# Kernel tuning notes

Hardware: AMD Instinct MI355X
Metric: run time of the kernel (lower is better)

## Reference

```python
import jax, jax.numpy as jnp
import numpy as np

B, S, D, H, V, DFF, L, MAXLEN = 256, 64, 1024, 16, 64, 4096, 8, 64
HD = D // H
SCALE = HD ** -0.5
EPS = 1e-5


def _ln(x, g, b):
    m = jnp.mean(x, axis=-1, keepdims=True)
    v = jnp.mean((x - m) ** 2, axis=-1, keepdims=True)
    return (x - m) * jax.lax.rsqrt(v + EPS) * g + b


def setup_inputs() -> dict:
    key = jax.random.key(0)
    ks = jax.random.split(key, 12)
    n = lambda k, shape: jax.random.normal(k, shape, jnp.float32) * 0.02
    return {
        "x": jax.random.randint(ks[0], (B, S), 0, V + 1),
        "step": 0,
        "token_embed": n(ks[1], (V + 1, D)),
        "step_embed": n(ks[2], (MAXLEN, D)),
        "qkv_w": n(ks[3], (L, 3 * D, D)),
        "qkv_b": jnp.zeros((L, 3 * D), jnp.float32),
        "out_w": n(ks[4], (L, D, D)),
        "out_b": jnp.zeros((L, D), jnp.float32),
        "rel_bias": n(ks[5], (L, 2 * MAXLEN - 1)),
        "w1": n(ks[6], (L, DFF, D)),
        "b1": jnp.zeros((L, DFF), jnp.float32),
        "w2": n(ks[7], (L, D, DFF)),
        "b2": jnp.zeros((L, D), jnp.float32),
        "ln1_g": jnp.ones((L, D), jnp.float32),
        "ln1_b": jnp.zeros((L, D), jnp.float32),
        "ln2_g": jnp.ones((L, D), jnp.float32),
        "ln2_b": jnp.zeros((L, D), jnp.float32),
        "lno_g": jnp.ones((D,), jnp.float32),
        "lno_b": jnp.zeros((D,), jnp.float32),
        "pol_w": n(ks[8], (V, D)),
        "pol_b": jnp.zeros((V,), jnp.float32),
        "val_w": n(ks[9], (1, D)),
        "val_b": jnp.zeros((1,), jnp.float32),
    }


def _forward(x, step, token_embed, step_embed, qkv_w, qkv_b, out_w, out_b,
             rel_bias, w1, b1, w2, b2, ln1_g, ln1_b, ln2_g, ln2_b,
             lno_g, lno_b, pol_w, pol_b, val_w, val_b):
    h = token_embed[x]  # [B,S,D]
    step_idx = min(int(step), MAXLEN - 1)
    h = h + step_embed[step_idx][None, None, :]

    pos = jnp.arange(S)
    rel_idx = jnp.clip(pos[:, None] - pos[None, :] + (MAXLEN - 1), 0, 2 * MAXLEN - 2)  # [S,S]

    def layer(h, p):
        qw, qb, ow, ob, rb, w1_, b1_, w2_, b2_, g1, be1, g2, be2 = p
        qkv = h @ qw.T + qb  # [B,S,3D]
        qkv = qkv.reshape(B, S, 3, H, HD).transpose(2, 0, 3, 1, 4)
        q, k, v = qkv[0], qkv[1], qkv[2]  # [B,H,S,HD]
        scores = jnp.einsum('bhqd,bhkd->bhqk', q, k) * SCALE + rb[rel_idx][None, None]
        probs = jax.nn.softmax(scores, axis=-1)
        attn = jnp.einsum('bhqk,bhkd->bhqd', probs, v)  # [B,H,S,HD]
        attn = attn.transpose(0, 2, 1, 3).reshape(B, S, D) @ ow.T + ob
        h = _ln(h + attn, g1, be1)
        ffn = jax.nn.gelu(h @ w1_.T + b1_, approximate=False) @ w2_.T + b2_
        h = _ln(h + ffn, g2, be2)
        return h, None

    h, _ = jax.lax.scan(layer, h, (qkv_w, qkv_b, out_w, out_b, rel_bias,
                                   w1, b1, w2, b2, ln1_g, ln1_b, ln2_g, ln2_b))
    h = _ln(h, lno_g, lno_b)
    pooled = h.mean(axis=1)  # [B,D]
    policy = pooled @ pol_w.T + pol_b  # [B,V]
    value = pooled @ val_w.T + val_b   # [B,1]
    return policy, value, h


def reference(x, step, token_embed, step_embed, qkv_w, qkv_b, out_w, out_b,
              rel_bias, w1, b1, w2, b2, ln1_g, ln1_b, ln2_g, ln2_b,
              lno_g, lno_b, pol_w, pol_b, val_w, val_b):
    return _forward(x, step, token_embed, step_embed, qkv_w, qkv_b, out_w, out_b,
                    rel_bias, w1, b1, w2, b2, ln1_g, ln1_b, ln2_g, ln2_b,
                    lno_g, lno_b, pol_w, pol_b, val_w, val_b)
```

## Files before the change

### kernel.cpp

```cpp
#include <hip/hip_runtime.h>
#include <math.h>

typedef _Float16 f16;
typedef _Float16 f16x8 __attribute__((ext_vector_type(8)));
typedef _Float16 f16x4 __attribute__((ext_vector_type(4)));
typedef float floatx4 __attribute__((ext_vector_type(4)));

#define BATCH 256
#define SEQ 64
#define DMODEL 1024
#define NHEAD 16
#define HDIM 64
#define VOCAB 64
#define DFF 4096
#define NLAYER 8
#define MS (BATCH*SEQ)

#define GPTR(p) ((const __attribute__((address_space(1))) void*)(p))
#define LPTR(p) ((__attribute__((address_space(3))) void*)(p))

__device__ __forceinline__ floatx4 mfma16(f16x8 a, f16x8 b, floatx4 c) {
    return __builtin_amdgcn_mfma_f32_16x16x32_f16(a, b, c, 0, 0, 0);
}

__device__ __forceinline__ float gelu_f(float x) {
    float x3 = x * x * x;
    float y = -1.5957691216f * fmaf(0.044715f, x3, x);
    return x / (1.f + __expf(y));
}

__global__ __launch_bounds__(256) void embed_k(const int* __restrict__ x, const int* __restrict__ step,
                                               const float* __restrict__ tok, const float* __restrict__ se,
                                               f16* __restrict__ r) {
    int row = blockIdx.x;
    int t = threadIdx.x;
    int id = x[row];
    int si = min(max(step[0], 0), 63);
    float4 a = ((const float4*)(tok + (size_t)id * DMODEL))[t];
    float4 b = ((const float4*)(se + (size_t)si * DMODEL))[t];
    f16x4 hv; hv[0] = (f16)(a.x + b.x); hv[1] = (f16)(a.y + b.y);
    hv[2] = (f16)(a.z + b.z); hv[3] = (f16)(a.w + b.w);
    ((f16x4*)(r + (size_t)row * DMODEL))[t] = hv;
}

__global__ __launch_bounds__(256) void cvt4_k(const float* __restrict__ qw, const float* __restrict__ ow,
                                              const float* __restrict__ w1, const float* __restrict__ w2,
                                              f16* __restrict__ dq, f16* __restrict__ dO,
                                              f16* __restrict__ d1, f16* __restrict__ d2) {
    int gid = blockIdx.x * 256 + threadIdx.x;
    const float4* s; f16x4* d; int off;
    if (gid < 786432)        { s = (const float4*)qw; d = (f16x4*)dq; off = gid; }
    else if (gid < 1048576)  { s = (const float4*)ow; d = (f16x4*)dO; off = gid - 786432; }
    else if (gid < 2097152)  { s = (const float4*)w1; d = (f16x4*)d1; off = gid - 1048576; }
    else                     { s = (const float4*)w2; d = (f16x4*)d2; off = gid - 2097152; }
    float4 v = s[off];
    f16x4 o; o[0] = (f16)v.x; o[1] = (f16)v.y; o[2] = (f16)v.z; o[3] = (f16)v.w;
    d[off] = o;
}

template<int MODE>
__global__ __launch_bounds__(256, 2) void gemm_k(const f16* __restrict__ A, const f16* __restrict__ Bw,
                                                 const float* __restrict__ bias,
                                                 f16* __restrict__ Cb,
                                                 const f16* __restrict__ Rres, f16* __restrict__ ResOut,
                                                 float2* __restrict__ Part,
                                                 int M, int N, int K) {
    __shared__ f16 smem[40960];

    const int tid = threadIdx.x;
    const int lane = tid & 63;
    const int wave = tid >> 6;
    const int wm = wave >> 1, wn = wave & 1;
    const int lr = lane & 15, lg = lane >> 4;
    const int sa = lr & 7;

    const unsigned nx = gridDim.x;
    const unsigned nwg = nx * gridDim.y;
    unsigned flat = blockIdx.y * nx + blockIdx.x;
    flat = (flat & 7u) * (nwg >> 3) + (flat >> 3);
    const int m0 = (int)(flat / nx) * 128;
    const int n0 = (int)(flat % nx) * 128;

    floatx4 acc[4][4] = {};

    const int srow = tid >> 3;
    const int scbs = (tid & 7) ^ (srow & 7);
    const f16* Asrc = A + (size_t)(m0 + srow) * K + scbs * 8;
    const f16* Bsrc = Bw + (size_t)(n0 + srow) * K + scbs * 8;
    const int ldsw = wave * 512;

#define STAGEA(bi, tt) do {                                                                       \
    const f16* _a = Asrc + (size_t)(tt) * 64;                                                     \
    f16* _l = smem + (bi) * 8192 + ldsw;                                                          \
    __builtin_amdgcn_global_load_lds(GPTR(_a),                  LPTR(_l),        16, 0, 0);       \
    __builtin_amdgcn_global_load_lds(GPTR(_a + 32 * (size_t)K), LPTR(_l + 2048), 16, 0, 0);       \
    __builtin_amdgcn_global_load_lds(GPTR(_a + 64 * (size_t)K), LPTR(_l + 4096), 16, 0, 0);       \
    __builtin_amdgcn_global_load_lds(GPTR(_a + 96 * (size_t)K), LPTR(_l + 6144), 16, 0, 0);       \
} while (0)

#define STAGEB(bi, tt) do {                                                                       \
    const f16* _b = Bsrc + (size_t)(tt) * 64;                                                     \
    f16* _l = smem + 16384 + (bi) * 8192 + ldsw;                                                  \
    __builtin_amdgcn_global_load_lds(GPTR(_b),                  LPTR(_l),        16, 0, 0);       \
    __builtin_amdgcn_global_load_lds(GPTR(_b + 32 * (size_t)K), LPTR(_l + 2048), 16, 0, 0);       \
    __builtin_amdgcn_global_load_lds(GPTR(_b + 64 * (size_t)K), LPTR(_l + 4096), 16, 0, 0);       \
    __builtin_amdgcn_global_load_lds(GPTR(_b + 96 * (size_t)K), LPTR(_l + 6144), 16, 0, 0);       \
} while (0)

    const int NT = K >> 6;

    STAGEA(0, 0);
    STAGEB(0, 0);
    STAGEB(1, 1);
    asm volatile("s_waitcnt vmcnt(4)" ::: "memory");
    __builtin_amdgcn_s_barrier();

    int ab = 0, bb = 0;
    for (int t = 0; t < NT; ++t) {
        if (t + 1 < NT) STAGEA(ab ^ 1, t + 1);
        if (t + 2 < NT) { int b2 = bb + 2; if (b2 >= 3) b2 -= 3; STAGEB(b2, t + 2); }

        const f16* Ab = smem + ab * 8192;
        const f16* Bb = smem + 16384 + bb * 8192;
        f16x8 af[8], bf[8];
#pragma unroll
        for (int kh = 0; kh < 2; ++kh)
#pragma unroll
            for (int mi = 0; mi < 4; ++mi)
                af[kh * 4 + mi] = *(const f16x8*)(Ab + (wm * 64 + mi * 16 + lr) * 64
                                                  + (((kh * 4 + lg) ^ sa) << 3));
#pragma unroll
        for (int kh = 0; kh < 2; ++kh)
#pragma unroll
            for (int ni = 0; ni < 4; ++ni)
                bf[kh * 4 + ni] = *(const f16x8*)(Bb + (wn * 64 + ni * 16 + lr) * 64
                                                  + (((kh * 4 + lg) ^ sa) << 3));

        __builtin_amdgcn_s_setprio(1);
#pragma unroll
        for (int kh = 0; kh < 2; ++kh)
#pragma unroll
            for (int mi = 0; mi < 4; ++mi)
#pragma unroll
                for (int ni = 0; ni < 4; ++ni)
                    acc[mi][ni] = mfma16(af[kh * 4 + mi], bf[kh * 4 + ni], acc[mi][ni]);
        __builtin_amdgcn_s_setprio(0);

        if (t + 2 < NT)      { asm volatile("s_waitcnt vmcnt(4)" ::: "memory"); }
        else if (t + 1 < NT) { asm volatile("s_waitcnt vmcnt(0)" ::: "memory"); }
        __builtin_amdgcn_s_barrier();

        ab ^= 1;
        bb = (bb == 2) ? 0 : bb + 1;
    }
#undef STAGEA
#undef STAGEB

    if (MODE == 2) {
        float bsv[4];
#pragma unroll
        for (int ni = 0; ni < 4; ++ni) bsv[ni] = bias[n0 + wn * 64 + ni * 16 + lr];
        f16* scr = smem + wave * 4096;
#pragma unroll
        for (int mi = 0; mi < 4; ++mi)
#pragma unroll
            for (int ni = 0; ni < 4; ++ni)
#pragma unroll
                for (int j = 0; j < 4; ++j) {
                    int rr = mi * 16 + lg * 4 + j;
                    int cc = ni * 16 + lr;
                    scr[rr * 64 + (((cc >> 3) ^ (rr & 7)) * 8) + (cc & 7)]
                        = (f16)(acc[mi][ni][j] + bsv[ni]);
                }
        int gr = m0 + wm * 64 + lane;
        const f16* rrow = Rres + (size_t)gr * N + n0 + wn * 64;
        f16* orow = ResOut + (size_t)gr * N + n0 + wn * 64;
        float s = 0.f, ss = 0.f;
#pragma unroll
        for (int i = 0; i < 8; ++i) {
            f16x8 a = *(const f16x8*)(scr + lane * 64 + ((i ^ (lane & 7)) * 8));
            f16x8 rv = *(const f16x8*)(rrow + i * 8);
            f16x8 o;
#pragma unroll
            for (int k = 0; k < 8; ++k) {
                float v = (float)a[k] + (float)rv[k];
                s += v; ss += v * v;
                o[k] = (f16)v;
            }
            *(f16x8*)(orow + i * 8) = o;
        }
        float* red = (float*)(smem + 16384);
        if (wn == 1) { red[(wm * 64 + lane) * 2] = s; red[(wm * 64 + lane) * 2 + 1] = ss; }
        __syncthreads();
        if (wn == 0) {
            float s2 = red[(wm * 64 + lane) * 2], ss2 = red[(wm * 64 + lane) * 2 + 1];
            Part[(size_t)gr * (N >> 7) + (n0 >> 7)] = float2{s + s2, ss + ss2};
        }
    } else {
        f16* scr = smem + wave * 4096;
        float bsv[4];
#pragma unroll
        for (int ni = 0; ni < 4; ++ni) bsv[ni] = bias[n0 + wn * 64 + ni * 16 + lr];
#pragma unroll
        for (int mi = 0; mi < 4; ++mi)
#pragma unroll
            for (int ni = 0; ni < 4; ++ni)
#pragma unroll
                for (int j = 0; j < 4; ++j) {
                    int rr = mi * 16 + lg * 4 + j;
                    int cc = ni * 16 + lr;
                    float v = acc[mi][ni][j] + bsv[ni];
                    if (MODE == 1) v = gelu_f(v);
                    scr[rr * 64 + (((cc >> 3) ^ (rr & 7)) * 8) + (cc & 7)] = (f16)v;
                }
        int gr = m0 + wm * 64 + lane;
        f16* dst = Cb + (size_t)gr * N + n0 + wn * 64;
#pragma unroll
        for (int i = 0; i < 8; ++i) {
            f16x8 v = *(const f16x8*)(scr + lane * 64 + ((i ^ (lane & 7)) * 8));
            *(f16x8*)(dst + i * 8) = v;
        }
    }
}

__global__ __launch_bounds__(64) void attn_k(const f16* __restrict__ qkv, const float* __restrict__ rb,
                                             f16* __restrict__ ctx) {
    const int hh = blockIdx.x;
    const int bb = blockIdx.y;
    const int lane = threadIdx.x;
    __shared__ float rbs[128];
    __shared__ f16 Vt[64][72];
    __shared__ f16 Pl[64][72];

    for (int i = lane; i < 127; i += 64) rbs[i] = rb[i];

    const f16* vrow = qkv + (size_t)(bb * 64 + lane) * 3072 + 2048 + hh * 64;
#pragma unroll
    for (int i = 0; i < 8; ++i) {
        f16x8 v = *(const f16x8*)(vrow + i * 8);
#pragma unroll
        for (int j = 0; j < 8; ++j) Vt[i * 8 + j][lane] = v[j];
    }
    __syncthreads();

    const int lr = lane & 15, lg = lane >> 4;
    floatx4 sacc[4][4] = {};
    const f16* qbase = qkv + (size_t)(bb * 64) * 3072 + hh * 64;
#pragma unroll
    for (int kk = 0; kk < 64; kk += 32) {
        f16x8 qa[4], kb[4];
#pragma unroll
        for (int mf = 0; mf < 4; ++mf)
            qa[mf] = *(const f16x8*)(qbase + (size_t)(mf * 16 + lr) * 3072 + kk + lg * 8);
#pragma unroll
        for (int nf = 0; nf < 4; ++nf)
            kb[nf] = *(const f16x8*)(qbase + 1024 + (size_t)(nf * 16 + lr) * 3072 + kk + lg * 8);
#pragma unroll
        for (int mf = 0; mf < 4; ++mf)
#pragma unroll
            for (int nf = 0; nf < 4; ++nf)
                sacc[mf][nf] = mfma16(qa[mf], kb[nf], sacc[mf][nf]);
    }

#pragma unroll
    for (int mf = 0; mf < 4; ++mf) {
#pragma unroll
        for (int j = 0; j < 4; ++j) {
            int qrow = mf * 16 + lg * 4 + j;
            float v0 = sacc[mf][0][j] * 0.125f + rbs[qrow - (0  + lr) + 63];
            float v1 = sacc[mf][1][j] * 0.125f + rbs[qrow - (16 + lr) + 63];
            float v2 = sacc[mf][2][j] * 0.125f + rbs[qrow - (32 + lr) + 63];
            float v3 = sacc[mf][3][j] * 0.125f + rbs[qrow - (48 + lr) + 63];
            float mx = fmaxf(fmaxf(v0, v1), fmaxf(v2, v3));
            for (int m = 1; m < 16; m <<= 1) mx = fmaxf(mx, __shfl_xor(mx, m));
            v0 = __expf(v0 - mx); v1 = __expf(v1 - mx); v2 = __expf(v2 - mx); v3 = __expf(v3 - mx);
            float sum = v0 + v1 + v2 + v3;
            for (int m = 1; m < 16; m <<= 1) sum += __shfl_xor(sum, m);
            float inv = 1.f / sum;
            Pl[qrow][0  + lr] = (f16)(v0 * inv);
            Pl[qrow][16 + lr] = (f16)(v1 * inv);
            Pl[qrow][32 + lr] = (f16)(v2 * inv);
            Pl[qrow][48 + lr] = (f16)(v3 * inv);
        }
    }
    __syncthreads();

    floatx4 oacc[4][4] = {};
#pragma unroll
    for (int kk = 0; kk < 64; kk += 32) {
        f16x8 pa[4], vb[4];
#pragma unroll
        for (int mf = 0; mf < 4; ++mf) pa[mf] = *(const f16x8*)&Pl[mf * 16 + lr][kk + lg * 8];
#pragma unroll
        for (int nf = 0; nf < 4; ++nf) vb[nf] = *(const f16x8*)&Vt[nf * 16 + lr][kk + lg * 8];
#pragma unroll
        for (int mf = 0; mf < 4; ++mf)
#pragma unroll
            for (int nf = 0; nf < 4; ++nf)
                oacc[mf][nf] = mfma16(pa[mf], vb[nf], oacc[mf][nf]);
    }
    __syncthreads();
#pragma unroll
    for (int mf = 0; mf < 4; ++mf)
#pragma unroll
        for (int nf = 0; nf < 4; ++nf)
#pragma unroll
            for (int j = 0; j < 4; ++j)
                Pl[mf * 16 + lg * 4 + j][nf * 16 + lr] = (f16)oacc[mf][nf][j];
    __syncthreads();
    f16* crow = ctx + (size_t)(bb * 64 + lane) * DMODEL + hh * 64;
#pragma unroll
    for (int i = 0; i < 8; ++i) {
        f16x8 v = *(const f16x8*)&Pl[lane][i * 8];
        *(f16x8*)(crow + i * 8) = v;
    }
}

__global__ __launch_bounds__(128) void ln_k(const f16* __restrict__ res, const float2* __restrict__ part,
                                            const float* __restrict__ g, const float* __restrict__ b,
                                            f16* __restrict__ out) {
    int row = blockIdx.x;
    int t = threadIdx.x;
    f16x8 rv = ((const f16x8*)(res + (size_t)row * DMODEL))[t];
    float s = 0.f, ss = 0.f;
#pragma unroll
    for (int c = 0; c < 8; ++c) {
        float2 p = part[(size_t)row * 8 + c];
        s += p.x; ss += p.y;
    }
    float mean = s * (1.f / 1024.f);
    float var = ss * (1.f / 1024.f) - mean * mean;
    float rstd = rsqrtf(var + 1e-5f);
    float4 g0 = ((const float4*)g)[t * 2], g1 = ((const float4*)g)[t * 2 + 1];
    float4 b0 = ((const float4*)b)[t * 2], b1 = ((const float4*)b)[t * 2 + 1];
    f16x8 o;
    o[0] = (f16)(((float)rv[0] - mean) * rstd * g0.x + b0.x);
    o[1] = (f16)(((float)rv[1] - mean) * rstd * g0.y + b0.y);
    o[2] = (f16)(((float)rv[2] - mean) * rstd * g0.z + b0.z);
    o[3] = (f16)(((float)rv[3] - mean) * rstd * g0.w + b0.w);
    o[4] = (f16)(((float)rv[4] - mean) * rstd * g1.x + b1.x);
    o[5] = (f16)(((float)rv[5] - mean) * rstd * g1.y + b1.y);
    o[6] = (f16)(((float)rv[6] - mean) * rstd * g1.z + b1.z);
    o[7] = (f16)(((float)rv[7] - mean) * rstd * g1.w + b1.w);
    ((f16x8*)(out + (size_t)row * DMODEL))[t] = o;
}

__global__ __launch_bounds__(256) void lnf_k(const f16* __restrict__ res, const float* __restrict__ g,
                                             const float* __restrict__ b, float* __restrict__ h) {
    int row = blockIdx.x;
    int t = threadIdx.x;
    f16x4 rv = ((const f16x4*)(res + (size_t)row * DMODEL))[t];
    float v0 = (float)rv[0], v1 = (float)rv[1], v2 = (float)rv[2], v3 = (float)rv[3];
    float s = v0 + v1 + v2 + v3;
    float ss = v0 * v0 + v1 * v1 + v2 * v2 + v3 * v3;
    for (int m = 1; m < 64; m <<= 1) { s += __shfl_xor(s, m); ss += __shfl_xor(ss, m); }
    __shared__ float red[8];
    if ((t & 63) == 0) { red[(t >> 6) * 2] = s; red[(t >> 6) * 2 + 1] = ss; }
    __syncthreads();
    s = red[0] + red[2] + red[4] + red[6];
    ss = red[1] + red[3] + red[5] + red[7];
    float mean = s * (1.f / 1024.f);
    float var = ss * (1.f / 1024.f) - mean * mean;
    float rstd = rsqrtf(var + 1e-5f);
    float4 gg = ((const float4*)g)[t];
    float4 bb = ((const float4*)b)[t];
    float4 o;
    o.x = (v0 - mean) * rstd * gg.x + bb.x;
    o.y = (v1 - mean) * rstd * gg.y + bb.y;
    o.z = (v2 - mean) * rstd * gg.z + bb.z;
    o.w = (v3 - mean) * rstd * gg.w + bb.w;
    ((float4*)(h + (size_t)row * DMODEL))[t] = o;
}

__global__ __launch_bounds__(256) void pool_k(const float* __restrict__ h, float* __restrict__ pooled) {
    int b = blockIdx.x;
    int t = threadIdx.x;
    float sx = 0, sy = 0, sz = 0, sw = 0;
    for (int s = 0; s < SEQ; ++s) {
        float4 v = ((const float4*)(h + (size_t)(b * SEQ + s) * DMODEL))[t];
        sx += v.x; sy += v.y; sz += v.z; sw += v.w;
    }
    float4 o; o.x = sx * (1.f / 64.f); o.y = sy * (1.f / 64.f); o.z = sz * (1.f / 64.f); o.w = sw * (1.f / 64.f);
    ((float4*)(pooled + (size_t)b * DMODEL))[t] = o;
}

__global__ __launch_bounds__(64) void head_k(const float* __restrict__ pooled, const float* __restrict__ pw,
                                             const float* __restrict__ pb, const float* __restrict__ vw,
                                             const float* __restrict__ vb, float* __restrict__ out) {
    int b = blockIdx.x;
    int lane = threadIdx.x;
    const float* pr = pooled + (size_t)b * DMODEL;
    const float* wr = pw + (size_t)lane * DMODEL;
    float accp = 0.f;
    for (int d = 0; d < DMODEL; d += 4) {
        float4 x = *(const float4*)(pr + d);
        float4 w = *(const float4*)(wr + d);
        accp += x.x * w.x + x.y * w.y + x.z * w.z + x.w * w.w;
    }
    float accv = 0.f;
    for (int d = lane * 4; d < DMODEL; d += 256) {
        float4 x = *(const float4*)(pr + d);
        float4 w = *(const float4*)(vw + d);
        accv += x.x * w.x + x.y * w.y + x.z * w.z + x.w * w.w;
    }
    for (int m = 1; m < 64; m <<= 1) accv += __shfl_xor(accv, m);
    out[b * VOCAB + lane] = accp + pb[lane];
    if (lane == 0) out[BATCH * VOCAB + b] = accv + vb[0];
}

extern "C" void kernel_launch(void* const* d_in, const int* in_sizes, int n_in,
                              void* d_out, int out_size, void* d_ws, size_t ws_size,
                              hipStream_t stream) {
    const int*   x      = (const int*)d_in[0];
    const int*   step   = (const int*)d_in[1];
    const float* tok    = (const float*)d_in[2];
    const float* se     = (const float*)d_in[3];
    const float* qkv_w  = (const float*)d_in[4];
    const float* qkv_b  = (const float*)d_in[5];
    const float* out_w  = (const float*)d_in[6];
    const float* out_b  = (const float*)d_in[7];
    const float* relb   = (const float*)d_in[8];
    const float* w1     = (const float*)d_in[9];
    const float* b1     = (const float*)d_in[10];
    const float* w2     = (const float*)d_in[11];
    const float* b2     = (const float*)d_in[12];
    const float* ln1g   = (const float*)d_in[13];
    const float* ln1b   = (const float*)d_in[14];
    const float* ln2g   = (const float*)d_in[15];
    const float* ln2b   = (const float*)d_in[16];
    const float* lnog   = (const float*)d_in[17];
    const float* lnob   = (const float*)d_in[18];
    const float* pw     = (const float*)d_in[19];
    const float* pb     = (const float*)d_in[20];
    const float* vw     = (const float*)d_in[21];
    const float* vb     = (const float*)d_in[22];

    float* out = (float*)d_out;
    float* h = out + BATCH * VOCAB + BATCH;

    char* ws = (char*)d_ws;
    f16* rB     = (f16*)(ws);
    f16* resA   = (f16*)(ws + 33554432);
    f16* qkv16  = (f16*)(ws + 67108864);
    f16* ctx16  = (f16*)(ws + 167772160);
    f16* ffn16  = (f16*)(ws + 67108864);
    f16* wqb    = (f16*)(ws + 201326592);
    f16* wob    = (f16*)(ws + 207618048);
    f16* w1b    = (f16*)(ws + 209715200);
    f16* w2b    = (f16*)(ws + 218103808);
    float2* part = (float2*)(ws + 226492416);
    float* pooled = (float*)(ws + 226492416);

    embed_k<<<MS, 256, 0, stream>>>(x, step, tok, se, rB);

    for (int l = 0; l < NLAYER; ++l) {
        cvt4_k<<<12288, 256, 0, stream>>>(qkv_w + (size_t)l * 3145728, out_w + (size_t)l * 1048576,
                                          w1 + (size_t)l * 4194304, w2 + (size_t)l * 4194304,
                                          wqb, wob, w1b, w2b);

        gemm_k<0><<<dim3(24, 128), 256, 0, stream>>>(rB, wqb, qkv_b + l * 3072, qkv16,
                                                     nullptr, nullptr, nullptr, MS, 3072, 1024);
        attn_k<<<dim3(NHEAD, BATCH), 64, 0, stream>>>(qkv16, relb + l * 127, ctx16);
        gemm_k<2><<<dim3(8, 128), 256, 0, stream>>>(ctx16, wob, out_b + l * 1024, nullptr,
                                                    rB, resA, part, MS, 1024, 1024);
        ln_k<<<MS, 128, 0, stream>>>(resA, part, ln1g + l * 1024, ln1b + l * 1024, rB);
        gemm_k<1><<<dim3(32, 128), 256, 0, stream>>>(rB, w1b, b1 + l * 4096, ffn16,
                                                     nullptr, nullptr, nullptr, MS, 4096, 1024);
        gemm_k<2><<<dim3(8, 128), 256, 0, stream>>>(ffn16, w2b, b2 + l * 1024, nullptr,
                                                    rB, resA, part, MS, 1024, 4096);
        ln_k<<<MS, 128, 0, stream>>>(resA, part, ln2g + l * 1024, ln2b + l * 1024, rB);
    }

    lnf_k<<<MS, 256, 0, stream>>>(rB, lnog, lnob, h);
    pool_k<<<BATCH, 256, 0, stream>>>(h, pooled);
    head_k<<<BATCH, 64, 0, stream>>>(pooled, pw, pb, vw, vb, out);
}
```

Baseline: 4.920 ms.

## Switch GEMM to 256x128 tiles with K=32 steps and unified triple-buffered staging

```diff
diff --git a/kernel.cpp b/kernel.cpp
--- a/kernel.cpp
+++ b/kernel.cpp
@@ -65,104 +65,84 @@
                                                  const f16* __restrict__ Rres, f16* __restrict__ ResOut,
                                                  float2* __restrict__ Part,
                                                  int M, int N, int K) {
-    __shared__ f16 smem[40960];
+    __shared__ f16 smem[36864];
 
     const int tid = threadIdx.x;
     const int lane = tid & 63;
     const int wave = tid >> 6;
     const int wm = wave >> 1, wn = wave & 1;
     const int lr = lane & 15, lg = lane >> 4;
-    const int sa = lr & 7;
+    const int sa = (lr ^ (lr >> 2)) & 3;
 
     const unsigned nx = gridDim.x;
     const unsigned nwg = nx * gridDim.y;
     unsigned flat = blockIdx.y * nx + blockIdx.x;
     flat = (flat & 7u) * (nwg >> 3) + (flat >> 3);
-    const int m0 = (int)(flat / nx) * 128;
+    const int m0 = (int)(flat / nx) * 256;
     const int n0 = (int)(flat % nx) * 128;
 
-    floatx4 acc[4][4] = {};
-
-    const int srow = tid >> 3;
-    const int scbs = (tid & 7) ^ (srow & 7);
-    const f16* Asrc = A + (size_t)(m0 + srow) * K + scbs * 8;
-    const f16* Bsrc = Bw + (size_t)(n0 + srow) * K + scbs * 8;
+    floatx4 acc[8][4] = {};
+
+    const int srow = tid >> 2;
+    const int lblk = (tid & 3) ^ ((srow ^ (srow >> 2)) & 3);
+    const f16* AsrcT = A + (size_t)(m0 + srow) * K + lblk * 8;
+    const f16* BsrcT = Bw + (size_t)(n0 + srow) * K + lblk * 8;
     const int ldsw = wave * 512;
 
-#define STAGEA(bi, tt) do {                                                                       \
-    const f16* _a = Asrc + (size_t)(tt) * 64;                                                     \
-    f16* _l = smem + (bi) * 8192 + ldsw;                                                          \
-    __builtin_amdgcn_global_load_lds(GPTR(_a),                  LPTR(_l),        16, 0, 0);       \
-    __builtin_amdgcn_global_load_lds(GPTR(_a + 32 * (size_t)K), LPTR(_l + 2048), 16, 0, 0);       \
-    __builtin_amdgcn_global_load_lds(GPTR(_a + 64 * (size_t)K), LPTR(_l + 4096), 16, 0, 0);       \
-    __builtin_amdgcn_global_load_lds(GPTR(_a + 96 * (size_t)K), LPTR(_l + 6144), 16, 0, 0);       \
+#define STAGE(bi, tt) do {                                                                        \
+    const f16* _a = AsrcT + (size_t)(tt) * 32;                                                    \
+    const f16* _b = BsrcT + (size_t)(tt) * 32;                                                    \
+    f16* _l = smem + (bi) * 12288 + ldsw;                                                         \
+    __builtin_amdgcn_global_load_lds(GPTR(_a),                   LPTR(_l),         16, 0, 0);     \
+    __builtin_amdgcn_global_load_lds(GPTR(_a +  64 * (size_t)K), LPTR(_l + 2048),  16, 0, 0);     \
+    __builtin_amdgcn_global_load_lds(GPTR(_a + 128 * (size_t)K), LPTR(_l + 4096),  16, 0, 0);     \
+    __builtin_amdgcn_global_load_lds(GPTR(_a + 192 * (size_t)K), LPTR(_l + 6144),  16, 0, 0);     \
+    __builtin_amdgcn_global_load_lds(GPTR(_b),                   LPTR(_l + 8192),  16, 0, 0);     \
+    __builtin_amdgcn_global_load_lds(GPTR(_b +  64 * (size_t)K), LPTR(_l + 10240), 16, 0, 0);     \
 } while (0)
 
-#define STAGEB(bi, tt) do {                                                                       \
-    const f16* _b = Bsrc + (size_t)(tt) * 64;                                                     \
-    f16* _l = smem + 16384 + (bi) * 8192 + ldsw;                                                  \
-    __builtin_amdgcn_global_load_lds(GPTR(_b),                  LPTR(_l),        16, 0, 0);       \
-    __builtin_amdgcn_global_load_lds(GPTR(_b + 32 * (size_t)K), LPTR(_l + 2048), 16, 0, 0);       \
-    __builtin_amdgcn_global_load_lds(GPTR(_b + 64 * (size_t)K), LPTR(_l + 4096), 16, 0, 0);       \
-    __builtin_amdgcn_global_load_lds(GPTR(_b + 96 * (size_t)K), LPTR(_l + 6144), 16, 0, 0);       \
-} while (0)
-
-    const int NT = K >> 6;
-
-    STAGEA(0, 0);
-    STAGEB(0, 0);
-    STAGEB(1, 1);
-    asm volatile("s_waitcnt vmcnt(4)" ::: "memory");
-    __builtin_amdgcn_s_barrier();
-
-    int ab = 0, bb = 0;
+    const int NT = K >> 5;
+
+    STAGE(0, 0);
+    STAGE(1, 1);
+
+    int buf = 0;
     for (int t = 0; t < NT; ++t) {
-        if (t + 1 < NT) STAGEA(ab ^ 1, t + 1);
-        if (t + 2 < NT) { int b2 = bb + 2; if (b2 >= 3) b2 -= 3; STAGEB(b2, t + 2); }
-
-        const f16* Ab = smem + ab * 8192;
-        const f16* Bb = smem + 16384 + bb * 8192;
-        f16x8 af[8], bf[8];
-#pragma unroll
-        for (int kh = 0; kh < 2; ++kh)
-#pragma unroll
-            for (int mi = 0; mi < 4; ++mi)
-                af[kh * 4 + mi] = *(const f16x8*)(Ab + (wm * 64 + mi * 16 + lr) * 64
-                                                  + (((kh * 4 + lg) ^ sa) << 3));
-#pragma unroll
-        for (int kh = 0; kh < 2; ++kh)
+        if (t + 1 < NT) { asm volatile("s_waitcnt vmcnt(6)" ::: "memory"); }
+        else            { asm volatile("s_waitcnt vmcnt(0)" ::: "memory"); }
+        __builtin_amdgcn_s_barrier();
+
+        if (t + 2 < NT) { int st = buf >= 1 ? buf - 1 : 2; STAGE(st, t + 2); }
+
+        const f16* Ab = smem + buf * 12288;
+        const f16* Bb = Ab + 8192;
+        f16x8 af[8], bf[4];
+#pragma unroll
+        for (int ni = 0; ni < 4; ++ni)
+            bf[ni] = *(const f16x8*)(Bb + (wn * 64 + ni * 16 + lr) * 32 + ((lg ^ sa) << 3));
+#pragma unroll
+        for (int mi = 0; mi < 8; ++mi)
+            af[mi] = *(const f16x8*)(Ab + (wm * 128 + mi * 16 + lr) * 32 + ((lg ^ sa) << 3));
+
+        __builtin_amdgcn_s_setprio(1);
+#pragma unroll
+        for (int mi = 0; mi < 8; ++mi)
 #pragma unroll
             for (int ni = 0; ni < 4; ++ni)
-                bf[kh * 4 + ni] = *(const f16x8*)(Bb + (wn * 64 + ni * 16 + lr) * 64
-                                                  + (((kh * 4 + lg) ^ sa) << 3));
-
-        __builtin_amdgcn_s_setprio(1);
-#pragma unroll
-        for (int kh = 0; kh < 2; ++kh)
-#pragma unroll
-            for (int mi = 0; mi < 4; ++mi)
-#pragma unroll
-                for (int ni = 0; ni < 4; ++ni)
-                    acc[mi][ni] = mfma16(af[kh * 4 + mi], bf[kh * 4 + ni], acc[mi][ni]);
+                acc[mi][ni] = mfma16(af[mi], bf[ni], acc[mi][ni]);
         __builtin_amdgcn_s_setprio(0);
 
-        if (t + 2 < NT)      { asm volatile("s_waitcnt vmcnt(4)" ::: "memory"); }
-        else if (t + 1 < NT) { asm volatile("s_waitcnt vmcnt(0)" ::: "memory"); }
-        __builtin_amdgcn_s_barrier();
-
-        ab ^= 1;
-        bb = (bb == 2) ? 0 : bb + 1;
-    }
-#undef STAGEA
-#undef STAGEB
+        buf = (buf == 2) ? 0 : buf + 1;
+    }
+#undef STAGE
 
     if (MODE == 2) {
         float bsv[4];
 #pragma unroll
         for (int ni = 0; ni < 4; ++ni) bsv[ni] = bias[n0 + wn * 64 + ni * 16 + lr];
-        f16* scr = smem + wave * 4096;
-#pragma unroll
-        for (int mi = 0; mi < 4; ++mi)
+        f16* scr = smem + wave * 8192;
+#pragma unroll
+        for (int mi = 0; mi < 8; ++mi)
 #pragma unroll
             for (int ni = 0; ni < 4; ++ni)
 #pragma unroll
@@ -172,37 +152,46 @@
                     scr[rr * 64 + (((cc >> 3) ^ (rr & 7)) * 8) + (cc & 7)]
                         = (f16)(acc[mi][ni][j] + bsv[ni]);
                 }
-        int gr = m0 + wm * 64 + lane;
-        const f16* rrow = Rres + (size_t)gr * N + n0 + wn * 64;
-        f16* orow = ResOut + (size_t)gr * N + n0 + wn * 64;
-        float s = 0.f, ss = 0.f;
-#pragma unroll
-        for (int i = 0; i < 8; ++i) {
-            f16x8 a = *(const f16x8*)(scr + lane * 64 + ((i ^ (lane & 7)) * 8));
-            f16x8 rv = *(const f16x8*)(rrow + i * 8);
-            f16x8 o;
-#pragma unroll
-            for (int k = 0; k < 8; ++k) {
-                float v = (float)a[k] + (float)rv[k];
-                s += v; ss += v * v;
-                o[k] = (f16)v;
+        float2* red = (float2*)(smem + 32768);
+#pragma unroll
+        for (int half = 0; half < 2; ++half) {
+            int r2 = half * 64 + lane;
+            int gr = m0 + wm * 128 + r2;
+            const f16* rrow = Rres + (size_t)gr * N + n0 + wn * 64;
+            f16* orow = ResOut + (size_t)gr * N + n0 + wn * 64;
+            float s = 0.f, ss = 0.f;
+#pragma unroll
+            for (int i = 0; i < 8; ++i) {
+                f16x8 a = *(const f16x8*)(scr + r2 * 64 + ((i ^ (r2 & 7)) * 8));
+                f16x8 rv = *(const f16x8*)(rrow + i * 8);
+                f16x8 o;
+#pragma unroll
+                for (int k = 0; k < 8; ++k) {
+                    float v = (float)a[k] + (float)rv[k];
+                    s += v; ss += v * v;
+                    o[k] = (f16)v;
+                }
+                *(f16x8*)(orow + i * 8) = o;
             }
-            *(f16x8*)(orow + i * 8) = o;
+            red[((wm * 128 + r2) << 1) | wn] = float2{s, ss};
         }
-        float* red = (float*)(smem + 16384);
-        if (wn == 1) { red[(wm * 64 + lane) * 2] = s; red[(wm * 64 + lane) * 2 + 1] = ss; }
         __syncthreads();
         if (wn == 0) {
-            float s2 = red[(wm * 64 + lane) * 2], ss2 = red[(wm * 64 + lane) * 2 + 1];
-            Part[(size_t)gr * (N >> 7) + (n0 >> 7)] = float2{s + s2, ss + ss2};
+#pragma unroll
+            for (int half = 0; half < 2; ++half) {
+                int row = wm * 128 + half * 64 + lane;
+                int gr = m0 + row;
+                float2 p0 = red[row << 1], p1 = red[(row << 1) | 1];
+                Part[(size_t)gr * (N >> 7) + (n0 >> 7)] = float2{p0.x + p1.x, p0.y + p1.y};
+            }
         }
     } else {
-        f16* scr = smem + wave * 4096;
+        f16* scr = smem + wave * 8192;
         float bsv[4];
 #pragma unroll
         for (int ni = 0; ni < 4; ++ni) bsv[ni] = bias[n0 + wn * 64 + ni * 16 + lr];
 #pragma unroll
-        for (int mi = 0; mi < 4; ++mi)
+        for (int mi = 0; mi < 8; ++mi)
 #pragma unroll
             for (int ni = 0; ni < 4; ++ni)
 #pragma unroll
@@ -213,12 +202,16 @@
                     if (MODE == 1) v = gelu_f(v);
                     scr[rr * 64 + (((cc >> 3) ^ (rr & 7)) * 8) + (cc & 7)] = (f16)v;
                 }
-        int gr = m0 + wm * 64 + lane;
-        f16* dst = Cb + (size_t)gr * N + n0 + wn * 64;
-#pragma unroll
-        for (int i = 0; i < 8; ++i) {
-            f16x8 v = *(const f16x8*)(scr + lane * 64 + ((i ^ (lane & 7)) * 8));
-            *(f16x8*)(dst + i * 8) = v;
+#pragma unroll
+        for (int half = 0; half < 2; ++half) {
+            int r2 = half * 64 + lane;
+            int gr = m0 + wm * 128 + r2;
+            f16* dst = Cb + (size_t)gr * N + n0 + wn * 64;
+#pragma unroll
+            for (int i = 0; i < 8; ++i) {
+                f16x8 v = *(const f16x8*)(scr + r2 * 64 + ((i ^ (r2 & 7)) * 8));
+                *(f16x8*)(dst + i * 8) = v;
+            }
         }
     }
 }
@@ -458,16 +451,16 @@
                                           w1 + (size_t)l * 4194304, w2 + (size_t)l * 4194304,
                                           wqb, wob, w1b, w2b);
 
-        gemm_k<0><<<dim3(24, 128), 256, 0, stream>>>(rB, wqb, qkv_b + l * 3072, qkv16,
-                                                     nullptr, nullptr, nullptr, MS, 3072, 1024);
+        gemm_k<0><<<dim3(24, 64), 256, 0, stream>>>(rB, wqb, qkv_b + l * 3072, qkv16,
+                                                    nullptr, nullptr, nullptr, MS, 3072, 1024);
         attn_k<<<dim3(NHEAD, BATCH), 64, 0, stream>>>(qkv16, relb + l * 127, ctx16);
-        gemm_k<2><<<dim3(8, 128), 256, 0, stream>>>(ctx16, wob, out_b + l * 1024, nullptr,
-                                                    rB, resA, part, MS, 1024, 1024);
+        gemm_k<2><<<dim3(8, 64), 256, 0, stream>>>(ctx16, wob, out_b + l * 1024, nullptr,
+                                                   rB, resA, part, MS, 1024, 1024);
         ln_k<<<MS, 128, 0, stream>>>(resA, part, ln1g + l * 1024, ln1b + l * 1024, rB);
-        gemm_k<1><<<dim3(32, 128), 256, 0, stream>>>(rB, w1b, b1 + l * 4096, ffn16,
-                                                     nullptr, nullptr, nullptr, MS, 4096, 1024);
-        gemm_k<2><<<dim3(8, 128), 256, 0, stream>>>(ffn16, w2b, b2 + l * 1024, nullptr,
-                                                    rB, resA, part, MS, 1024, 4096);
+        gemm_k<1><<<dim3(32, 64), 256, 0, stream>>>(rB, w1b, b1 + l * 4096, ffn16,
+                                                    nullptr, nullptr, nullptr, MS, 4096, 1024);
+        gemm_k<2><<<dim3(8, 64), 256, 0, stream>>>(ffn16, w2b, b2 + l * 1024, nullptr,
+                                                   rB, resA, part, MS, 1024, 4096);
         ln_k<<<MS, 128, 0, stream>>>(resA, part, ln2g + l * 1024, ln2b + l * 1024, rB);
     }
 
```

After: 4.860 ms. No clear change (-1.2%).

## Add 256x256-tile 8-wave GEMM for QKV and FFN-up projections

Applied to the files above, without the earlier changes.

```diff
diff --git a/kernel.cpp b/kernel.cpp
--- a/kernel.cpp
+++ b/kernel.cpp
@@ -18,6 +18,8 @@
 
 #define GPTR(p) ((const __attribute__((address_space(1))) void*)(p))
 #define LPTR(p) ((__attribute__((address_space(3))) void*)(p))
+#define GLDS(s, d) __builtin_amdgcn_global_load_lds(GPTR(s), LPTR(d), 16, 0, 0)
+#define BARR() asm volatile("s_barrier" ::: "memory")
 
 __device__ __forceinline__ floatx4 mfma16(f16x8 a, f16x8 b, floatx4 c) {
     return __builtin_amdgcn_mfma_f32_16x16x32_f16(a, b, c, 0, 0, 0);
@@ -59,12 +61,149 @@
 }
 
 template<int MODE>
-__global__ __launch_bounds__(256, 2) void gemm_k(const f16* __restrict__ A, const f16* __restrict__ Bw,
-                                                 const float* __restrict__ bias,
-                                                 f16* __restrict__ Cb,
-                                                 const f16* __restrict__ Rres, f16* __restrict__ ResOut,
-                                                 float2* __restrict__ Part,
-                                                 int M, int N, int K) {
+__global__ __launch_bounds__(512, 2) void gemm8_k(const f16* __restrict__ A, const f16* __restrict__ Bw,
+                                                  const float* __restrict__ bias, f16* __restrict__ Cb,
+                                                  int M, int N, int K) {
+    __shared__ f16 smem[65536];
+
+    const int tid = threadIdx.x;
+    const int lane = tid & 63;
+    const int wave = tid >> 6;
+    const int wm = wave >> 2, wn = wave & 3;
+    const int lr = lane & 15, lg = lane >> 4;
+    const int sa = lr & 7;
+
+    const unsigned nx = gridDim.x;
+    const unsigned nwg = nx * gridDim.y;
+    unsigned flat = blockIdx.y * nx + blockIdx.x;
+    flat = (flat & 7u) * (nwg >> 3) + (flat >> 3);
+    const int m0 = (int)(flat / nx) * 256;
+    const int n0 = (int)(flat % nx) * 256;
+
+    floatx4 acc[8][4] = {};
+
+    const int srow = tid >> 3;
+    const int scb = (tid & 7) ^ (srow & 7);
+    const f16* Ag = A + (size_t)(m0 + srow) * K + scb * 8;
+    const f16* Bg = Bw + (size_t)(n0 + srow) * K + scb * 8;
+    const int ldsw = wave * 512;
+
+#define STAGE_A(bi, tt) do { const f16* _p = Ag + (size_t)(tt) * 64;                       \
+    f16* _d = smem + (bi) * 32768 + ldsw;                                                  \
+    GLDS(_p, _d); GLDS(_p + 64 * (size_t)K, _d + 4096);                                    \
+    GLDS(_p + 128 * (size_t)K, _d + 8192); GLDS(_p + 192 * (size_t)K, _d + 12288); } while (0)
+#define STAGE_BH(bi, tt, h) do { const f16* _p = Bg + (size_t)(tt) * 64 + (size_t)(h) * 128 * K; \
+    f16* _d = smem + (bi) * 32768 + 16384 + (h) * 8192 + ldsw;                             \
+    GLDS(_p, _d); GLDS(_p + 64 * (size_t)K, _d + 4096); } while (0)
+
+    const int NT = K >> 6;
+
+    STAGE_A(0, 0);
+    STAGE_BH(0, 0, 0); STAGE_BH(0, 0, 1);
+    STAGE_BH(1, 1, 0); STAGE_BH(1, 1, 1);
+    asm volatile("s_waitcnt vmcnt(4)" ::: "memory");
+    BARR();
+
+    for (int t = 0; t < NT; ++t) {
+        const int pofs = (t & 1) << 15;
+        const f16* Ab = smem + pofs;
+        const f16* Bb = smem + pofs + 16384;
+        f16x8 bf[4][2];
+
+        {
+            f16x8 af[2][2];
+#pragma unroll
+            for (int kh = 0; kh < 2; ++kh)
+#pragma unroll
+                for (int i = 0; i < 2; ++i)
+                    af[i][kh] = *(const f16x8*)(Ab + (wm * 128 + i * 16 + lr) * 64 + (((kh * 4 + lg) ^ sa) << 3));
+#pragma unroll
+            for (int kh = 0; kh < 2; ++kh)
+#pragma unroll
+                for (int ni = 0; ni < 4; ++ni)
+                    bf[ni][kh] = *(const f16x8*)(Bb + (wn * 64 + ni * 16 + lr) * 64 + (((kh * 4 + lg) ^ sa) << 3));
+            if (t + 1 < NT) STAGE_A((t & 1) ^ 1, t + 1);
+            asm volatile("s_waitcnt lgkmcnt(8)" ::: "memory");
+            BARR();
+            asm volatile("s_waitcnt lgkmcnt(0)" ::: "memory");
+            __builtin_amdgcn_sched_barrier(0);
+            __builtin_amdgcn_s_setprio(1);
+#pragma unroll
+            for (int kh = 0; kh < 2; ++kh)
+#pragma unroll
+                for (int i = 0; i < 2; ++i)
+#pragma unroll
+                    for (int ni = 0; ni < 4; ++ni)
+                        acc[i][ni] = mfma16(af[i][kh], bf[ni][kh], acc[i][ni]);
+            __builtin_amdgcn_s_setprio(0);
+            BARR();
+        }
+#pragma unroll
+        for (int q = 1; q < 4; ++q) {
+            f16x8 af[2][2];
+#pragma unroll
+            for (int kh = 0; kh < 2; ++kh)
+#pragma unroll
+                for (int i = 0; i < 2; ++i)
+                    af[i][kh] = *(const f16x8*)(Ab + (wm * 128 + q * 32 + i * 16 + lr) * 64 + (((kh * 4 + lg) ^ sa) << 3));
+            if (q == 1 && t + 2 < NT) STAGE_BH(t & 1, t + 2, 0);
+            if (q == 2 && t + 2 < NT) STAGE_BH(t & 1, t + 2, 1);
+            BARR();
+            asm volatile("s_waitcnt lgkmcnt(0)" ::: "memory");
+            __builtin_amdgcn_sched_barrier(0);
+            __builtin_amdgcn_s_setprio(1);
+#pragma unroll
+            for (int kh = 0; kh < 2; ++kh)
+#pragma unroll
+                for (int i = 0; i < 2; ++i)
+#pragma unroll
+                    for (int ni = 0; ni < 4; ++ni)
+                        acc[q * 2 + i][ni] = mfma16(af[i][kh], bf[ni][kh], acc[q * 2 + i][ni]);
+            __builtin_amdgcn_s_setprio(0);
+            if (q == 3) {
+                if (t + 2 < NT)      { asm volatile("s_waitcnt vmcnt(4)" ::: "memory"); }
+                else if (t + 1 < NT) { asm volatile("s_waitcnt vmcnt(0)" ::: "memory"); }
+            }
+            BARR();
+        }
+    }
+#undef STAGE_A
+#undef STAGE_BH
+
+    f16* scr = smem + wave * 8192;
+    float bsv[4];
+#pragma unroll
+    for (int ni = 0; ni < 4; ++ni) bsv[ni] = bias[n0 + wn * 64 + ni * 16 + lr];
+#pragma unroll
+    for (int mi = 0; mi < 8; ++mi)
+#pragma unroll
+        for (int ni = 0; ni < 4; ++ni)
+#pragma unroll
+            for (int j = 0; j < 4; ++j) {
+                int rr = mi * 16 + lg * 4 + j;
+                int cc = ni * 16 + lr;
+                float v = acc[mi][ni][j] + bsv[ni];
+                if (MODE == 1) v = gelu_f(v);
+                scr[rr * 64 + (((cc >> 3) ^ (rr & 7)) * 8) + (cc & 7)] = (f16)v;
+            }
+#pragma unroll
+    for (int half = 0; half < 2; ++half) {
+        int r2 = half * 64 + lane;
+        int gr = m0 + wm * 128 + r2;
+        f16* dst = Cb + (size_t)gr * N + n0 + wn * 64;
+#pragma unroll
+        for (int i = 0; i < 8; ++i) {
+            f16x8 v = *(const f16x8*)(scr + r2 * 64 + ((i ^ (r2 & 7)) * 8));
+            *(f16x8*)(dst + i * 8) = v;
+        }
+    }
+}
+
+__global__ __launch_bounds__(256, 2) void gemm2_k(const f16* __restrict__ A, const f16* __restrict__ Bw,
+                                                  const float* __restrict__ bias,
+                                                  const f16* __restrict__ Rres, f16* __restrict__ ResOut,
+                                                  float2* __restrict__ Part,
+                                                  int M, int N, int K) {
     __shared__ f16 smem[40960];
 
     const int tid = threadIdx.x;
@@ -89,23 +228,14 @@
     const f16* Bsrc = Bw + (size_t)(n0 + srow) * K + scbs * 8;
     const int ldsw = wave * 512;
 
-#define STAGEA(bi, tt) do {                                                                       \
-    const f16* _a = Asrc + (size_t)(tt) * 64;                                                     \
-    f16* _l = smem + (bi) * 8192 + ldsw;                                                          \
-    __builtin_amdgcn_global_load_lds(GPTR(_a),                  LPTR(_l),        16, 0, 0);       \
-    __builtin_amdgcn_global_load_lds(GPTR(_a + 32 * (size_t)K), LPTR(_l + 2048), 16, 0, 0);       \
-    __builtin_amdgcn_global_load_lds(GPTR(_a + 64 * (size_t)K), LPTR(_l + 4096), 16, 0, 0);       \
-    __builtin_amdgcn_global_load_lds(GPTR(_a + 96 * (size_t)K), LPTR(_l + 6144), 16, 0, 0);       \
-} while (0)
-
-#define STAGEB(bi, tt) do {                                                                       \
-    const f16* _b = Bsrc + (size_t)(tt) * 64;                                                     \
-    f16* _l = smem + 16384 + (bi) * 8192 + ldsw;                                                  \
-    __builtin_amdgcn_global_load_lds(GPTR(_b),                  LPTR(_l),        16, 0, 0);       \
-    __builtin_amdgcn_global_load_lds(GPTR(_b + 32 * (size_t)K), LPTR(_l + 2048), 16, 0, 0);       \
-    __builtin_amdgcn_global_load_lds(GPTR(_b + 64 * (size_t)K), LPTR(_l + 4096), 16, 0, 0);       \
-    __builtin_amdgcn_global_load_lds(GPTR(_b + 96 * (size_t)K), LPTR(_l + 6144), 16, 0, 0);       \
-} while (0)
+#define STAGEA(bi, tt) do { const f16* _a = Asrc + (size_t)(tt) * 64;                      \
+    f16* _l = smem + (bi) * 8192 + ldsw;                                                   \
+    GLDS(_a, _l); GLDS(_a + 32 * (size_t)K, _l + 2048);                                    \
+    GLDS(_a + 64 * (size_t)K, _l + 4096); GLDS(_a + 96 * (size_t)K, _l + 6144); } while (0)
+#define STAGEB(bi, tt) do { const f16* _b = Bsrc + (size_t)(tt) * 64;                      \
+    f16* _l = smem + 16384 + (bi) * 8192 + ldsw;                                           \
+    GLDS(_b, _l); GLDS(_b + 32 * (size_t)K, _l + 2048);                                    \
+    GLDS(_b + 64 * (size_t)K, _l + 4096); GLDS(_b + 96 * (size_t)K, _l + 6144); } while (0)
 
     const int NT = K >> 6;
 
@@ -156,70 +286,44 @@
 #undef STAGEA
 #undef STAGEB
 
-    if (MODE == 2) {
-        float bsv[4];
-#pragma unroll
-        for (int ni = 0; ni < 4; ++ni) bsv[ni] = bias[n0 + wn * 64 + ni * 16 + lr];
-        f16* scr = smem + wave * 4096;
-#pragma unroll
-        for (int mi = 0; mi < 4; ++mi)
-#pragma unroll
-            for (int ni = 0; ni < 4; ++ni)
-#pragma unroll
-                for (int j = 0; j < 4; ++j) {
-                    int rr = mi * 16 + lg * 4 + j;
-                    int cc = ni * 16 + lr;
-                    scr[rr * 64 + (((cc >> 3) ^ (rr & 7)) * 8) + (cc & 7)]
-                        = (f16)(acc[mi][ni][j] + bsv[ni]);
-                }
-        int gr = m0 + wm * 64 + lane;
-        const f16* rrow = Rres + (size_t)gr * N + n0 + wn * 64;
-        f16* orow = ResOut + (size_t)gr * N + n0 + wn * 64;
-        float s = 0.f, ss = 0.f;
-#pragma unroll
-        for (int i = 0; i < 8; ++i) {
-            f16x8 a = *(const f16x8*)(scr + lane * 64 + ((i ^ (lane & 7)) * 8));
-            f16x8 rv = *(const f16x8*)(rrow + i * 8);
-            f16x8 o;
-#pragma unroll
-            for (int k = 0; k < 8; ++k) {
-                float v = (float)a[k] + (float)rv[k];
-                s += v; ss += v * v;
-                o[k] = (f16)v;
+    float bsv[4];
+#pragma unroll
+    for (int ni = 0; ni < 4; ++ni) bsv[ni] = bias[n0 + wn * 64 + ni * 16 + lr];
+    f16* scr = smem + wave * 4096;
+#pragma unroll
+    for (int mi = 0; mi < 4; ++mi)
+#pragma unroll
+        for (int ni = 0; ni < 4; ++ni)
+#pragma unroll
+            for (int j = 0; j < 4; ++j) {
+                int rr = mi * 16 + lg * 4 + j;
+                int cc = ni * 16 + lr;
+                scr[rr * 64 + (((cc >> 3) ^ (rr & 7)) * 8) + (cc & 7)]
+                    = (f16)(acc[mi][ni][j] + bsv[ni]);
             }
-            *(f16x8*)(orow + i * 8) = o;
+    int gr = m0 + wm * 64 + lane;
+    const f16* rrow = Rres + (size_t)gr * N + n0 + wn * 64;
+    f16* orow = ResOut + (size_t)gr * N + n0 + wn * 64;
+    float s = 0.f, ss = 0.f;
+#pragma unroll
+    for (int i = 0; i < 8; ++i) {
+        f16x8 a = *(const f16x8*)(scr + lane * 64 + ((i ^ (lane & 7)) * 8));
+        f16x8 rv = *(const f16x8*)(rrow + i * 8);
+        f16x8 o;
+#pragma unroll
+        for (int k = 0; k < 8; ++k) {
+            float v = (float)a[k] + (float)rv[k];
+            s += v; ss += v * v;
+            o[k] = (f16)v;
         }
-        float* red = (float*)(smem + 16384);
-        if (wn == 1) { red[(wm * 64 + lane) * 2] = s; red[(wm * 64 + lane) * 2 + 1] = ss; }
-        __syncthreads();
-        if (wn == 0) {
-            float s2 = red[(wm * 64 + lane) * 2], ss2 = red[(wm * 64 + lane) * 2 + 1];
-            Part[(size_t)gr * (N >> 7) + (n0 >> 7)] = float2{s + s2, ss + ss2};
-        }
-    } else {
-        f16* scr = smem + wave * 4096;
-        float bsv[4];
-#pragma unroll
-        for (int ni = 0; ni < 4; ++ni) bsv[ni] = bias[n0 + wn * 64 + ni * 16 + lr];
-#pragma unroll
-        for (int mi = 0; mi < 4; ++mi)
-#pragma unroll
-            for (int ni = 0; ni < 4; ++ni)
-#pragma unroll
-                for (int j = 0; j < 4; ++j) {
-                    int rr = mi * 16 + lg * 4 + j;
-                    int cc = ni * 16 + lr;
-                    float v = acc[mi][ni][j] + bsv[ni];
-                    if (MODE == 1) v = gelu_f(v);
-                    scr[rr * 64 + (((cc >> 3) ^ (rr & 7)) * 8) + (cc & 7)] = (f16)v;
-                }
-        int gr = m0 + wm * 64 + lane;
-        f16* dst = Cb + (size_t)gr * N + n0 + wn * 64;
-#pragma unroll
-        for (int i = 0; i < 8; ++i) {
-            f16x8 v = *(const f16x8*)(scr + lane * 64 + ((i ^ (lane & 7)) * 8));
-            *(f16x8*)(dst + i * 8) = v;
-        }
+        *(f16x8*)(orow + i * 8) = o;
+    }
+    float* red = (float*)(smem + 16384);
+    if (wn == 1) { red[(wm * 64 + lane) * 2] = s; red[(wm * 64 + lane) * 2 + 1] = ss; }
+    __syncthreads();
+    if (wn == 0) {
+        float s2 = red[(wm * 64 + lane) * 2], ss2 = red[(wm * 64 + lane) * 2 + 1];
+        Part[(size_t)gr * (N >> 7) + (n0 >> 7)] = float2{s + s2, ss + ss2};
     }
 }
 
@@ -458,16 +562,14 @@
                                           w1 + (size_t)l * 4194304, w2 + (size_t)l * 4194304,
                                           wqb, wob, w1b, w2b);
 
-        gemm_k<0><<<dim3(24, 128), 256, 0, stream>>>(rB, wqb, qkv_b + l * 3072, qkv16,
-                                                     nullptr, nullptr, nullptr, MS, 3072, 1024);
+        gemm8_k<0><<<dim3(12, 64), 512, 0, stream>>>(rB, wqb, qkv_b + l * 3072, qkv16, MS, 3072, 1024);
         attn_k<<<dim3(NHEAD, BATCH), 64, 0, stream>>>(qkv16, relb + l * 127, ctx16);
-        gemm_k<2><<<dim3(8, 128), 256, 0, stream>>>(ctx16, wob, out_b + l * 1024, nullptr,
-                                                    rB, resA, part, MS, 1024, 1024);
+        gemm2_k<<<dim3(8, 128), 256, 0, stream>>>(ctx16, wob, out_b + l * 1024,
+                                                  rB, resA, part, MS, 1024, 1024);
         ln_k<<<MS, 128, 0, stream>>>(resA, part, ln1g + l * 1024, ln1b + l * 1024, rB);
-        gemm_k<1><<<dim3(32, 128), 256, 0, stream>>>(rB, w1b, b1 + l * 4096, ffn16,
-                                                     nullptr, nullptr, nullptr, MS, 4096, 1024);
-        gemm_k<2><<<dim3(8, 128), 256, 0, stream>>>(ffn16, w2b, b2 + l * 1024, nullptr,
-                                                    rB, resA, part, MS, 1024, 4096);
+        gemm8_k<1><<<dim3(16, 64), 512, 0, stream>>>(rB, w1b, b1 + l * 4096, ffn16, MS, 4096, 1024);
+        gemm2_k<<<dim3(8, 128), 256, 0, stream>>>(ffn16, w2b, b2 + l * 1024,
+                                                  rB, resA, part, MS, 1024, 4096);
         ln_k<<<MS, 128, 0, stream>>>(resA, part, ln2g + l * 1024, ln2b + l * 1024, rB);
     }
 
```

New measurement: 4.675 ms, median of 3. 5.0% less time.
